# Kernel optimization log

Measured on AMD Instinct MI355X. Metric: run time of the kernel, lower is better.

## Reference

```python
import jax, jax.numpy as jnp
import numpy as np


def setup_inputs() -> dict:
    key = jax.random.key(0)
    k1, k2 = jax.random.split(key)
    B, P, N, C = 2048, 64, 64, 10
    x = jax.random.normal(k1, (B, P, N), dtype=jnp.float32)
    weight = 0.1 * jax.random.normal(k2, (C, P * N), dtype=jnp.float32)
    return {"x": x, "weight": weight}


def reference(x, weight):
    # x: (B, P, N) -> flatten to (B, F) with F = P*N
    B = x.shape[0]
    xf = x.reshape(B, -1)                      # (B, F)
    w = jax.nn.log_softmax(weight, axis=1)     # (C, F)
    # log-space matmul: logsumexp over F of x[b,f] + w[c,f]
    out = jax.scipy.special.logsumexp(xf[:, None, :] + w[None, :, :], axis=-1)  # (B, C)
    return out
```

## Files before the change

### kernel.cpp

```cpp
#include <hip/hip_runtime.h>
#include <math.h>

#define FEAT 4096
#define NC   10
#define ROWS 2
#define BLK  256
#define F4   (FEAT/4)
#define ITERS (F4/BLK)

__global__ __launch_bounds__(BLK) void fused_kernel(const float* __restrict__ x,
                                                    const float* __restrict__ weight,
                                                    float* __restrict__ out) {
    const int t  = threadIdx.x;
    const int b0 = blockIdx.x * ROWS;
    const float4* xv = (const float4*)x;
    const float4* wv = (const float4*)weight;

    float acc[ROWS][NC];
#pragma unroll
    for (int r = 0; r < ROWS; ++r)
#pragma unroll
        for (int c = 0; c < NC; ++c) acc[r][c] = 0.f;
    float sew[NC];
#pragma unroll
    for (int c = 0; c < NC; ++c) sew[c] = 0.f;

#pragma unroll
    for (int k = 0; k < ITERS; ++k) {
        const int i = k * BLK + t;
        float ex[ROWS][4];
#pragma unroll
        for (int r = 0; r < ROWS; ++r) {
            float4 x4 = xv[(size_t)(b0 + r) * F4 + i];
            ex[r][0] = __expf(x4.x); ex[r][1] = __expf(x4.y);
            ex[r][2] = __expf(x4.z); ex[r][3] = __expf(x4.w);
        }
#pragma unroll
        for (int c = 0; c < NC; ++c) {
            float4 w4 = wv[(size_t)c * F4 + i];
            w4.x = __expf(w4.x); w4.y = __expf(w4.y);
            w4.z = __expf(w4.z); w4.w = __expf(w4.w);
            sew[c] += (w4.x + w4.y) + (w4.z + w4.w);
#pragma unroll
            for (int r = 0; r < ROWS; ++r) {
                acc[r][c] = fmaf(ex[r][0], w4.x, acc[r][c]);
                acc[r][c] = fmaf(ex[r][1], w4.y, acc[r][c]);
                acc[r][c] = fmaf(ex[r][2], w4.z, acc[r][c]);
                acc[r][c] = fmaf(ex[r][3], w4.w, acc[r][c]);
            }
        }
    }

    __shared__ float red[4][ROWS * NC];
    __shared__ float redw[4][NC];
    const int wave = t >> 6;
    const int lane = t & 63;

#pragma unroll
    for (int r = 0; r < ROWS; ++r)
#pragma unroll
        for (int c = 0; c < NC; ++c) {
            float v = acc[r][c];
#pragma unroll
            for (int off = 32; off >= 1; off >>= 1) v += __shfl_xor(v, off, 64);
            acc[r][c] = v;
        }
#pragma unroll
    for (int c = 0; c < NC; ++c) {
        float v = sew[c];
#pragma unroll
        for (int off = 32; off >= 1; off >>= 1) v += __shfl_xor(v, off, 64);
        sew[c] = v;
    }
    if (lane == 0) {
#pragma unroll
        for (int r = 0; r < ROWS; ++r)
#pragma unroll
            for (int c = 0; c < NC; ++c) red[wave][r * NC + c] = acc[r][c];
#pragma unroll
        for (int c = 0; c < NC; ++c) redw[wave][c] = sew[c];
    }
    __syncthreads();
    if (t < ROWS * NC) {
        const int r = t / NC, c = t % NC;
        float v = red[0][t] + red[1][t] + red[2][t] + red[3][t];
        float s = redw[0][c] + redw[1][c] + redw[2][c] + redw[3][c];
        out[(size_t)(b0 + r) * NC + c] = __logf(v) - __logf(s);
    }
}

extern "C" void kernel_launch(void* const* d_in, const int* in_sizes, int n_in,
                              void* d_out, int out_size, void* d_ws, size_t ws_size,
                              hipStream_t stream) {
    const float* x      = (const float*)d_in[0];
    const float* weight = (const float*)d_in[1];
    float*       out    = (float*)d_out;

    const int B = in_sizes[0] / FEAT;
    const int grid = B / ROWS;

    fused_kernel<<<grid, BLK, 0, stream>>>(x, weight, out);
}
```

Baseline: 90.59 us.

## Precompute exp(weight) and its log-sum in a prep kernel, widen main blocks

Adds a small prep kernel that computes exp(weight) and the per-class log-sum-exp once into workspace, so the main kernel no longer recomputes weight exponentials and sums in every block. The main kernel now processes 4 rows per 512-thread block, which halves the grid and spreads weight reads over more rows. The cost is an extra kernel launch and serialisation on a tiny 10-block prep kernel, plus more accumulator registers per thread. Like the original, it uses unstabilised exp without max subtraction.

```diff
diff --git a/kernel.cpp b/kernel.cpp
--- a/kernel.cpp
+++ b/kernel.cpp
@@ -3,27 +3,55 @@
 
 #define FEAT 4096
 #define NC   10
-#define ROWS 2
-#define BLK  256
-#define F4   (FEAT/4)
-#define ITERS (F4/BLK)
 
-__global__ __launch_bounds__(BLK) void fused_kernel(const float* __restrict__ x,
-                                                    const float* __restrict__ weight,
-                                                    float* __restrict__ out) {
+#define PBLK 256
+#define PITERS (FEAT / 4 / PBLK)
+
+__global__ __launch_bounds__(PBLK) void prep_kernel(const float* __restrict__ weight,
+                                                    float* __restrict__ ew,
+                                                    float* __restrict__ lse) {
+    int c = blockIdx.x;
+    int t = threadIdx.x;
+    const float4* wv  = (const float4*)(weight + (size_t)c * FEAT);
+    float4*       ewv = (float4*)(ew + (size_t)c * FEAT);
+    float s = 0.f;
+#pragma unroll
+    for (int k = 0; k < PITERS; ++k) {
+        float4 w4 = wv[k * PBLK + t];
+        float4 e4;
+        e4.x = __expf(w4.x); e4.y = __expf(w4.y);
+        e4.z = __expf(w4.z); e4.w = __expf(w4.w);
+        ewv[k * PBLK + t] = e4;
+        s += (e4.x + e4.y) + (e4.z + e4.w);
+    }
+#pragma unroll
+    for (int off = 32; off >= 1; off >>= 1) s += __shfl_xor(s, off, 64);
+    __shared__ float ls[PBLK / 64];
+    if ((t & 63) == 0) ls[t >> 6] = s;
+    __syncthreads();
+    if (t == 0) lse[c] = __logf(ls[0] + ls[1] + ls[2] + ls[3]);
+}
+
+#define BLK  512
+#define ROWS 4
+#define F4   (FEAT / 4)
+#define ITERS (F4 / BLK)
+#define NWAVE (BLK / 64)
+
+__global__ __launch_bounds__(BLK) void main_kernel(const float* __restrict__ x,
+                                                   const float* __restrict__ ew,
+                                                   const float* __restrict__ lse,
+                                                   float* __restrict__ out) {
     const int t  = threadIdx.x;
     const int b0 = blockIdx.x * ROWS;
     const float4* xv = (const float4*)x;
-    const float4* wv = (const float4*)weight;
+    const float4* wv = (const float4*)ew;
 
     float acc[ROWS][NC];
 #pragma unroll
     for (int r = 0; r < ROWS; ++r)
 #pragma unroll
         for (int c = 0; c < NC; ++c) acc[r][c] = 0.f;
-    float sew[NC];
-#pragma unroll
-    for (int c = 0; c < NC; ++c) sew[c] = 0.f;
 
 #pragma unroll
     for (int k = 0; k < ITERS; ++k) {
@@ -38,9 +66,6 @@
 #pragma unroll
         for (int c = 0; c < NC; ++c) {
             float4 w4 = wv[(size_t)c * F4 + i];
-            w4.x = __expf(w4.x); w4.y = __expf(w4.y);
-            w4.z = __expf(w4.z); w4.w = __expf(w4.w);
-            sew[c] += (w4.x + w4.y) + (w4.z + w4.w);
 #pragma unroll
             for (int r = 0; r < ROWS; ++r) {
                 acc[r][c] = fmaf(ex[r][0], w4.x, acc[r][c]);
@@ -51,8 +76,7 @@
         }
     }
 
-    __shared__ float red[4][ROWS * NC];
-    __shared__ float redw[4][NC];
+    __shared__ float red[NWAVE][ROWS * NC];
     const int wave = t >> 6;
     const int lane = t & 63;
 
@@ -65,27 +89,19 @@
             for (int off = 32; off >= 1; off >>= 1) v += __shfl_xor(v, off, 64);
             acc[r][c] = v;
         }
-#pragma unroll
-    for (int c = 0; c < NC; ++c) {
-        float v = sew[c];
-#pragma unroll
-        for (int off = 32; off >= 1; off >>= 1) v += __shfl_xor(v, off, 64);
-        sew[c] = v;
-    }
     if (lane == 0) {
 #pragma unroll
         for (int r = 0; r < ROWS; ++r)
 #pragma unroll
             for (int c = 0; c < NC; ++c) red[wave][r * NC + c] = acc[r][c];
-#pragma unroll
-        for (int c = 0; c < NC; ++c) redw[wave][c] = sew[c];
     }
     __syncthreads();
     if (t < ROWS * NC) {
         const int r = t / NC, c = t % NC;
-        float v = red[0][t] + red[1][t] + red[2][t] + red[3][t];
-        float s = redw[0][c] + redw[1][c] + redw[2][c] + redw[3][c];
-        out[(size_t)(b0 + r) * NC + c] = __logf(v) - __logf(s);
+        float v = 0.f;
+#pragma unroll
+        for (int w = 0; w < NWAVE; ++w) v += red[w][t];
+        out[(size_t)(b0 + r) * NC + c] = __logf(v) - lse[c];
     }
 }
 
@@ -99,5 +115,8 @@
     const int B = in_sizes[0] / FEAT;
     const int grid = B / ROWS;
 
-    fused_kernel<<<grid, BLK, 0, stream>>>(x, weight, out);
+    float* ew  = (float*)d_ws;
+    float* lse = (float*)((char*)d_ws + (size_t)NC * FEAT * sizeof(float));
+    prep_kernel<<<NC, PBLK, 0, stream>>>(weight, ew, lse);
+    main_kernel<<<grid, BLK, 0, stream>>>(x, ew, lse, out);
 }
```

Result: faster. 85.24 us (-5.9%).
